# Optimization experiments

Hardware: AMD Instinct MI355X
Metric: run time of the kernel (lower is better)

The kernel has to match this reference:

```python
import jax, jax.numpy as jnp
import numpy as np

B, L = 32, 65536
N_FILTERS, K = 8, 8
THR, BETA, DT, X_SCALE, GAIN = 0.25, 15.0, 1.0, 20.0, 1.0
RAW_TAU0 = float(np.log(np.expm1(3.0)))
RAW_GAIN0 = float(np.log(np.expm1(1.0)))


def setup_inputs() -> dict:
    key = jax.random.key(0)
    kx, ka, kb = jax.random.split(key, 3)
    return {
        "x": jax.random.normal(kx, (B, 2, L), dtype=jnp.float32),
        "wa": jax.random.normal(ka, (N_FILTERS, 1, K), dtype=jnp.float32) * 0.3,
        "wb": jax.random.normal(kb, (N_FILTERS, 1, K), dtype=jnp.float32) * 0.3,
        "raw_tau_a": jnp.full((N_FILTERS,), RAW_TAU0, dtype=jnp.float32),
        "raw_tau_b": jnp.full((N_FILTERS,), RAW_TAU0, dtype=jnp.float32),
        "raw_gain_a": jnp.asarray(RAW_GAIN0, dtype=jnp.float32),
        "raw_gain_b": jnp.asarray(RAW_GAIN0, dtype=jnp.float32),
    }


def causal_conv(x, w):
    # x: (B,1,L), w: (C,1,K); weight rows normalized to unit L2 norm
    norms = jnp.clip(jnp.linalg.norm(w.reshape(w.shape[0], -1), axis=1), 1e-8, None)
    wn = w / norms[:, None, None]
    return jax.lax.conv_general_dilated(
        x, wn, window_strides=(1,), padding=[(w.shape[2] - 1, 0)],
        dimension_numbers=("NCH", "OIH", "NCH"))


def lif(I, raw_tau):
    # I: (B,C,L); explicit per-timestep LIF dynamics as a lax.scan
    dtype = I.dtype
    alpha = jnp.exp(-DT / (jax.nn.softplus(raw_tau) + 1e-4)).astype(dtype)  # (C,)
    thr = jnp.asarray(THR, dtype)

    def step(v, I_t):
        v_pre = alpha * v + (1 - alpha) * I_t
        z = BETA * (v_pre - thr)
        s = (v_pre >= thr).astype(dtype)  # non-differentiable spike, matches torch
        return v_pre * (1 - s), (z, s)

    I_tbc = jnp.moveaxis(I, 2, 0)  # (L,B,C)
    v0 = jnp.zeros(I.shape[:2], dtype)
    _, (z, s) = jax.lax.scan(step, v0, I_tbc)
    return jnp.moveaxis(z, 0, 2), jnp.moveaxis(s, 0, 2)  # (B,C,L)


def reference(x, wa, wb, raw_tau_a, raw_tau_b, raw_gain_a, raw_gain_b):
    ga = jax.nn.softplus(raw_gain_a) + 1e-4
    gb = jax.nn.softplus(raw_gain_b) + 1e-4
    Ia = GAIN * ga * causal_conv(X_SCALE * x[:, 0:1], wa)
    Ib = GAIN * gb * causal_conv(X_SCALE * x[:, 1:2], wb)
    za, sa = lif(Ia, raw_tau_a)
    zb, sb = lif(Ib, raw_tau_b)
    I = jnp.concatenate([Ia, Ib], axis=1)
    z = jnp.concatenate([za, zb], axis=1)
    s = jnp.concatenate([sa, sb], axis=1)
    logits = jnp.max(z, axis=1)  # (B,L)
    return I, z, s, logits
```

## Files before the change

### kernel.cpp

```cpp
#include <hip/hip_runtime.h>
#include <math.h>

#define LL    65536
#define NB    32
#define TSUB  128
#define TBLK  (16 * TSUB)
#define NTILES (LL / TBLK)
#define WARM  192
#define NI    (NB * 16 * LL)

__device__ __forceinline__ double softplus_d(double x) {
  return (x > 0.0) ? (x + log1p(exp(-x))) : log1p(exp(x));
}

__global__ __launch_bounds__(256, 4)
void snn_fused(const float* __restrict__ x,
               const float* __restrict__ wa, const float* __restrict__ wb,
               const float* __restrict__ rta, const float* __restrict__ rtb,
               const float* __restrict__ rga, const float* __restrict__ rgb,
               float* __restrict__ out)
{
  const int tid  = threadIdx.x;
  const int c16  = tid & 15;
  const int j    = tid >> 4;
  const int tile = blockIdx.x;
  const int b    = blockIdx.y;
  const int br   = c16 >> 3;
  const int c    = c16 & 7;

  const float* wrow = (br ? wb : wa) + c * 8;
  double ss = 0.0;
  #pragma unroll
  for (int k = 0; k < 8; ++k) { double wv = (double)wrow[k]; ss += wv * wv; }
  double nrm = sqrt(ss); if (nrm < 1e-8) nrm = 1e-8;
  const float w0 = (float)((double)wrow[0] / nrm);
  const float w1 = (float)((double)wrow[1] / nrm);
  const float w2 = (float)((double)wrow[2] / nrm);
  const float w3 = (float)((double)wrow[3] / nrm);
  const float w4 = (float)((double)wrow[4] / nrm);
  const float w5 = (float)((double)wrow[5] / nrm);
  const float w6 = (float)((double)wrow[6] / nrm);
  const float w7 = (float)((double)wrow[7] / nrm);

  const float rt    = br ? rtb[c] : rta[c];
  const float alpha = (float)exp(-1.0 / (softplus_d((double)rt) + 1e-4));
  const float oma   = 1.0f - alpha;
  const float g     = (float)(softplus_d((double)(br ? rgb[0] : rga[0])) + 1e-4);

  const int t_out = tile * TBLK + j * TSUB;
  int t0 = t_out - WARM; if (t0 < 0) t0 = 0;

  const float* xrow = x + (size_t)(b * 2 + br) * LL;

  float m7, m6, m5, m4, m3, m2, m1;
  {
    const int base = t0 - 7;
    m7 = (base + 0 >= 0) ? 20.0f * xrow[base + 0] : 0.0f;
    m6 = (base + 1 >= 0) ? 20.0f * xrow[base + 1] : 0.0f;
    m5 = (base + 2 >= 0) ? 20.0f * xrow[base + 2] : 0.0f;
    m4 = (base + 3 >= 0) ? 20.0f * xrow[base + 3] : 0.0f;
    m3 = (base + 4 >= 0) ? 20.0f * xrow[base + 4] : 0.0f;
    m2 = (base + 5 >= 0) ? 20.0f * xrow[base + 5] : 0.0f;
    m1 = (base + 6 >= 0) ? 20.0f * xrow[base + 6] : 0.0f;
  }
  float v = 0.0f;

  auto step = [&](float cx, float& Iv, float& zv) {
    float acc = m7 * w0;
    acc = fmaf(m6, w1, acc);
    acc = fmaf(m5, w2, acc);
    acc = fmaf(m4, w3, acc);
    acc = fmaf(m3, w4, acc);
    acc = fmaf(m2, w5, acc);
    acc = fmaf(m1, w6, acc);
    acc = fmaf(cx, w7, acc);
    Iv = g * acc;
    float vpre = fmaf(alpha, v, oma * Iv);
    zv = 15.0f * (vpre - 0.25f);
    v  = (vpre >= 0.25f) ? 0.0f : vpre;
    m7 = m6; m6 = m5; m5 = m4; m4 = m3; m3 = m2; m2 = m1; m1 = cx;
  };

  for (int t = t0; t < t_out; t += 4) {
    const float4 xv = *(const float4*)(xrow + t);
    float dI, dz;
    step(20.0f * xv.x, dI, dz);
    step(20.0f * xv.y, dI, dz);
    step(20.0f * xv.z, dI, dz);
    step(20.0f * xv.w, dI, dz);
  }

  float* outI = out + (size_t)(b * 16 + c16) * LL;
  float* outZ = outI + (size_t)NI;
  float* outS = outI + (size_t)2 * NI;
  float* outG = out + (size_t)3 * NI + (size_t)b * LL;

  for (int t = t_out; t < t_out + TSUB; t += 32) {
    float Ib[32], zb[32];
    #pragma unroll
    for (int q = 0; q < 8; ++q) {
      const float4 xv = *(const float4*)(xrow + t + 4 * q);
      step(20.0f * xv.x, Ib[4*q+0], zb[4*q+0]);
      step(20.0f * xv.y, Ib[4*q+1], zb[4*q+1]);
      step(20.0f * xv.z, Ib[4*q+2], zb[4*q+2]);
      step(20.0f * xv.w, Ib[4*q+3], zb[4*q+3]);
    }

    float4* pI = (float4*)(outI + t);
    float4* pZ = (float4*)(outZ + t);
    float4* pS = (float4*)(outS + t);
    #pragma unroll
    for (int q = 0; q < 8; ++q)
      pI[q] = make_float4(Ib[4*q+0], Ib[4*q+1], Ib[4*q+2], Ib[4*q+3]);
    #pragma unroll
    for (int q = 0; q < 8; ++q)
      pZ[q] = make_float4(zb[4*q+0], zb[4*q+1], zb[4*q+2], zb[4*q+3]);
    #pragma unroll
    for (int q = 0; q < 8; ++q)
      pS[q] = make_float4(zb[4*q+0] >= 0.0f ? 1.0f : 0.0f,
                          zb[4*q+1] >= 0.0f ? 1.0f : 0.0f,
                          zb[4*q+2] >= 0.0f ? 1.0f : 0.0f,
                          zb[4*q+3] >= 0.0f ? 1.0f : 0.0f);

    #pragma unroll
    for (int msk = 1; msk < 16; msk <<= 1) {
      #pragma unroll
      for (int q = 0; q < 32; ++q) zb[q] = fmaxf(zb[q], __shfl_xor(zb[q], msk, 16));
    }
    if (c16 == 0) {
      float4* pG = (float4*)(outG + t);
      #pragma unroll
      for (int q = 0; q < 8; ++q)
        pG[q] = make_float4(zb[4*q+0], zb[4*q+1], zb[4*q+2], zb[4*q+3]);
    }
  }
}

extern "C" void kernel_launch(void* const* d_in, const int* in_sizes, int n_in,
                              void* d_out, int out_size, void* d_ws, size_t ws_size,
                              hipStream_t stream) {
  const float* x   = (const float*)d_in[0];
  const float* wa  = (const float*)d_in[1];
  const float* wb  = (const float*)d_in[2];
  const float* rta = (const float*)d_in[3];
  const float* rtb = (const float*)d_in[4];
  const float* rga = (const float*)d_in[5];
  const float* rgb = (const float*)d_in[6];
  float* out = (float*)d_out;

  dim3 grid(NTILES, NB);
  hipLaunchKernelGGL(snn_fused, grid, dim3(256), 0, stream,
                     x, wa, wb, rta, rtb, rga, rgb, out);
}
```

Measured before the change: 545.0 us.

## Transpose output tiles through LDS for coalesced global stores

Output writes for I, z and s are staged through a per-wave shared-memory buffer, padded to 36 floats per row, and re-read in a transposed pattern. Each store instruction then writes contiguous 128-byte segments per channel row, instead of each lane writing its own scattered 128-float span. This targets poor store coalescing on a write-bound kernel. The cost is extra LDS traffic, no explicit barrier between the LDS writes and reads (it relies on wave-level lockstep), and 36 KB of shared memory per block, which may reduce occupancy.

```diff
diff --git a/kernel.cpp b/kernel.cpp
--- a/kernel.cpp
+++ b/kernel.cpp
@@ -90,12 +90,20 @@
     step(20.0f * xv.w, dI, dz);
   }
 
-  float* outI = out + (size_t)(b * 16 + c16) * LL;
-  float* outZ = outI + (size_t)NI;
-  float* outS = outI + (size_t)2 * NI;
+  __shared__ __align__(16) float xp[4][64 * 36];
+  const int lane = tid & 63;
+  const int wv   = tid >> 6;
+  const int hi   = lane >> 3;
+  const int lo   = lane & 7;
+  float*       lrow = &xp[wv][lane * 36];
+  const float* lrd  = &xp[wv][hi * 288 + 4 * lo];
+  const int gbase = (b * 16 + 8 * (hi & 1)) * LL
+                  + tile * TBLK + (wv * 4 + (hi >> 1)) * TSUB + 4 * lo;
+
   float* outG = out + (size_t)3 * NI + (size_t)b * LL;
 
   for (int t = t_out; t < t_out + TSUB; t += 32) {
+    const int bb = t - t_out + (gbase - 0);
     float Ib[32], zb[32];
     #pragma unroll
     for (int q = 0; q < 8; ++q) {
@@ -106,21 +114,35 @@
       step(20.0f * xv.w, Ib[4*q+3], zb[4*q+3]);
     }
 
-    float4* pI = (float4*)(outI + t);
-    float4* pZ = (float4*)(outZ + t);
-    float4* pS = (float4*)(outS + t);
     #pragma unroll
     for (int q = 0; q < 8; ++q)
-      pI[q] = make_float4(Ib[4*q+0], Ib[4*q+1], Ib[4*q+2], Ib[4*q+3]);
+      *(float4*)(lrow + 4 * q) = make_float4(Ib[4*q+0], Ib[4*q+1], Ib[4*q+2], Ib[4*q+3]);
+    #pragma unroll
+    for (int r = 0; r < 8; ++r) {
+      const float4 v4 = *(const float4*)(lrd + 36 * r);
+      *(float4*)(out + (size_t)(bb + r * LL)) = v4;
+    }
+
     #pragma unroll
     for (int q = 0; q < 8; ++q)
-      pZ[q] = make_float4(zb[4*q+0], zb[4*q+1], zb[4*q+2], zb[4*q+3]);
+      *(float4*)(lrow + 4 * q) = make_float4(zb[4*q+0], zb[4*q+1], zb[4*q+2], zb[4*q+3]);
+    #pragma unroll
+    for (int r = 0; r < 8; ++r) {
+      const float4 v4 = *(const float4*)(lrd + 36 * r);
+      *(float4*)(out + (size_t)NI + (size_t)(bb + r * LL)) = v4;
+    }
+
     #pragma unroll
     for (int q = 0; q < 8; ++q)
-      pS[q] = make_float4(zb[4*q+0] >= 0.0f ? 1.0f : 0.0f,
-                          zb[4*q+1] >= 0.0f ? 1.0f : 0.0f,
-                          zb[4*q+2] >= 0.0f ? 1.0f : 0.0f,
-                          zb[4*q+3] >= 0.0f ? 1.0f : 0.0f);
+      *(float4*)(lrow + 4 * q) = make_float4(zb[4*q+0] >= 0.0f ? 1.0f : 0.0f,
+                                             zb[4*q+1] >= 0.0f ? 1.0f : 0.0f,
+                                             zb[4*q+2] >= 0.0f ? 1.0f : 0.0f,
+                                             zb[4*q+3] >= 0.0f ? 1.0f : 0.0f);
+    #pragma unroll
+    for (int r = 0; r < 8; ++r) {
+      const float4 v4 = *(const float4*)(lrd + 36 * r);
+      *(float4*)(out + (size_t)2 * NI + (size_t)(bb + r * LL)) = v4;
+    }
 
     #pragma unroll
     for (int msk = 1; msk < 16; msk <<= 1) {
```

After: 456.8 us. -16.2%, faster.
